# Optimization experiments

Measured on AMD Instinct MI355X. Metric: run time of the kernel, lower is better.

Reference implementation:

```python
import jax, jax.numpy as jnp
import numpy as np

IN_C, HID_C, OUT_C = 6, 128, 6
B, H, W = 8, 256, 256


def _make_weight(key, oc, ic):
    return jax.random.normal(key, (oc, ic, 5), dtype=jnp.float32) / np.sqrt(ic * 5)


def setup_inputs() -> dict:
    key = jax.random.key(0)
    ks = jax.random.split(key, 5)
    x = jax.random.normal(ks[0], (B, IN_C, H, W), dtype=jnp.float32)
    return {
        "x": x,
        "w1": _make_weight(ks[1], HID_C, IN_C),
        "b1": jnp.zeros((HID_C,), jnp.float32),
        "w2": _make_weight(ks[2], HID_C, HID_C),
        "b2": jnp.zeros((HID_C,), jnp.float32),
        "w3": _make_weight(ks[3], HID_C, HID_C),
        "b3": jnp.zeros((HID_C,), jnp.float32),
        "w4": _make_weight(ks[4], OUT_C, HID_C),
        "b4": jnp.zeros((OUT_C,), jnp.float32),
    }


def cross_conv(x, w, b):
    # w: [oc, ic, 5] -> dense 3x3 kernel with 5-point cross stencil
    oc, ic, _ = w.shape
    k = jnp.zeros((oc, ic, 3, 3), dtype=w.dtype)
    k = k.at[:, :, 1, 1].set(w[:, :, 0])  # center
    k = k.at[:, :, 0, 1].set(w[:, :, 1])  # up
    k = k.at[:, :, 2, 1].set(w[:, :, 2])  # down
    k = k.at[:, :, 1, 0].set(w[:, :, 3])  # left
    k = k.at[:, :, 1, 2].set(w[:, :, 4])  # right
    y = jax.lax.conv_general_dilated(
        x, k, window_strides=(1, 1), padding="SAME",
        dimension_numbers=("NCHW", "OIHW", "NCHW"))
    return y + b[None, :, None, None]


def reference(x, w1, b1, w2, b2, w3, b3, w4, b4):
    h = jax.nn.relu(cross_conv(x, w1, b1))
    h = jax.nn.relu(cross_conv(h, w2, b2))
    h = jax.nn.relu(cross_conv(h, w3, b3))
    return cross_conv(h, w4, b4)
```

## Files before the change

kernel.cpp:

```cpp
#include <hip/hip_runtime.h>


#define BB   8
#define HH   256
#define WW   256

typedef _Float16 f16x8 __attribute__((ext_vector_type(8)));
typedef float    f32x4 __attribute__((ext_vector_type(4)));

__device__ _Float16 W1g[128 * 32];
__device__ _Float16 W2g[20 * 128 * 32];
__device__ _Float16 W3g[20 * 128 * 32];
__device__ _Float16 W4g[5 * 16 * 128];

__global__ void prep(const float* __restrict__ w1, const float* __restrict__ w2,
                     const float* __restrict__ w3, const float* __restrict__ w4)
{
    int idx = blockIdx.x * 256 + threadIdx.x;
    if (idx < 81920) {
        int icb = idx & 31, oc = (idx >> 5) & 127, ks = idx >> 12;
        int tap = ks >> 2, ic = (ks & 3) * 32 + icb;
        W2g[idx] = (_Float16)w2[(oc * 128 + ic) * 5 + tap];
    } else if (idx < 163840) {
        int k = idx - 81920;
        int icb = k & 31, oc = (k >> 5) & 127, ks = k >> 12;
        int tap = ks >> 2, ic = (ks & 3) * 32 + icb;
        W3g[k] = (_Float16)w3[(oc * 128 + ic) * 5 + tap];
    } else if (idx < 174080) {
        int k = idx - 163840;
        int t = k / 2048, oc = (k >> 7) & 15, ic = k & 127;
        W4g[k] = (_Float16)((oc < 6) ? w4[(oc * 128 + ic) * 5 + t] : 0.f);
    } else if (idx < 178176) {
        int k = idx - 174080;
        int kk = k & 31, oc = k >> 5;
        float v = 0.f;
        if (kk < 30) {
            int tap = (kk * 43) >> 8;
            int ic = kk - 6 * tap;
            v = w1[(oc * 6 + ic) * 5 + tap];
        }
        W1g[k] = (_Float16)v;
    }
}

template<int HALF, bool EDGE>
__device__ __forceinline__ void g1_stage(const float* __restrict__ xb,
                                         _Float16* __restrict__ Ap,
                                         int px, int gi0, int gj0)
{
#pragma unroll
    for (int it = 0; it < 15; ++it) {
        const int k = 2 * it + HALF;
        const int tap = k / 6, ic = k - 6 * tap;
        const int DI = (tap == 1) ? -1 : ((tap == 2) ? 1 : 0);
        const int DJ = (tap == 3) ? -1 : ((tap == 4) ? 1 : 0);
        const float* sp = xb + ic * 65536 + DI * 256 + DJ;
        float v;
        if (EDGE) {
            const int gi = gi0 + DI, gj = gj0 + DJ;
            v = ((unsigned)gi < 256u && (unsigned)gj < 256u) ? *sp : 0.f;
        } else {
            v = *sp;
        }
        Ap[px * 40 + k] = (_Float16)v;
    }
    Ap[px * 40 + 30 + HALF] = (_Float16)0.f;
}

__global__ __launch_bounds__(256, 3) void g1(
    const float* __restrict__ x, const float* __restrict__ bias,
    _Float16* __restrict__ outp)
{
    __shared__ _Float16 Ap[128 * 40];
    const int tid = threadIdx.x;
    const int j0 = blockIdx.x * 16, i0 = blockIdx.y * 8, b = blockIdx.z;
    const int px = tid & 127, half = tid >> 7;
    const int pr = px >> 4, pp = px & 15;
    const bool edge = (blockIdx.y == 0) | (blockIdx.y == 31) |
                      (blockIdx.x == 0) | (blockIdx.x == 15);
    const int gi0 = i0 + pr, gj0 = j0 + pp;
    const float* xb = x + (size_t)b * 6 * 65536 + gi0 * 256 + gj0;

    if (edge) {
        if (half == 0) g1_stage<0, true >(xb, Ap, px, gi0, gj0);
        else           g1_stage<1, true >(xb, Ap, px, gi0, gj0);
    } else {
        if (half == 0) g1_stage<0, false>(xb, Ap, px, gi0, gj0);
        else           g1_stage<1, false>(xb, Ap, px, gi0, gj0);
    }
    __syncthreads();

    const int lane = tid & 63, w = tid >> 6, l16 = lane & 15, quad = lane >> 4;
    f32x4 acc[2][8] = {};
    f16x8 a0 = *(const f16x8*)&Ap[((2 * w + 0) * 16 + l16) * 40 + quad * 8];
    f16x8 a1 = *(const f16x8*)&Ap[((2 * w + 1) * 16 + l16) * 40 + quad * 8];
#pragma unroll
    for (int nf = 0; nf < 8; ++nf) {
        f16x8 bf = *(const f16x8*)&W1g[(nf * 16 + l16) * 32 + quad * 8];
        acc[0][nf] = __builtin_amdgcn_mfma_f32_16x16x32_f16(a0, bf, acc[0][nf], 0, 0, 0);
        acc[1][nf] = __builtin_amdgcn_mfma_f32_16x16x32_f16(a1, bf, acc[1][nf], 0, 0, 0);
    }
#pragma unroll
    for (int mf = 0; mf < 2; ++mf) {
        const size_t rowb = ((size_t)b * 256 + i0 + 2 * w + mf) * 256 + j0;
#pragma unroll
        for (int nf = 0; nf < 8; ++nf) {
            const float bv = bias[nf * 16 + l16];
#pragma unroll
            for (int r = 0; r < 4; ++r)
                outp[(rowb + quad * 4 + r) * 128 + nf * 16 + l16] =
                    (_Float16)fmaxf(acc[mf][nf][r] + bv, 0.f);
        }
    }
}

template<int LAYER>
__global__ __launch_bounds__(256, 3) void gmid(
    const _Float16* __restrict__ in, const float* __restrict__ bias,
    _Float16* __restrict__ outp)
{
    const _Float16* wt = (LAYER == 2) ? W2g : W3g;
    __shared__ __align__(16) _Float16 Al[180 * 128];
    const int tid = threadIdx.x;
    const int lane = tid & 63, w = tid >> 6;
    const int j0 = blockIdx.x * 16, i0 = blockIdx.y * 8, b = blockIdx.z;
    const bool top = (blockIdx.y == 0), bot = (blockIdx.y == 31);
    const bool left = (blockIdx.x == 0), right = (blockIdx.x == 15);

    {
        const int pxl = lane & 15;
#pragma unroll
        for (int k = 0; k < 12; ++k) {
            const int m = w + 4 * k;
            if (m < 45) {
                const int s = 4 * m + (lane >> 4);
                const int r = (s * 114) >> 11;
                const int p = s - 18 * r;
                int gi = i0 - 1 + r; gi = gi < 0 ? 0 : (gi > 255 ? 255 : gi);
                int gj = j0 - 1 + p; gj = gj < 0 ? 0 : (gj > 255 ? 255 : gj);
                const _Float16* src = in + (((size_t)(b * 256 + gi)) * 256 + gj) * 128
                                         + ((pxl ^ (s & 7)) << 3);
                __builtin_amdgcn_global_load_lds(
                    (const __attribute__((address_space(1))) void*)src,
                    (__attribute__((address_space(3))) void*)(Al + m * 512),
                    16, 0, 0);
            }
        }
    }
    __syncthreads();
    if (top | bot | left | right) {
#pragma unroll
        for (int pass = 0; pass < 2; ++pass) {
            const int gidx = (tid >> 3) + 32 * pass, c = tid & 7;
            int sid = -1;
            if (gidx < 18)      { if (top)   sid = gidx; }
            else if (gidx < 36) { if (bot)   sid = 162 + gidx - 18; }
            else if (gidx < 46) { if (left)  sid = (gidx - 36) * 18; }
            else if (gidx < 56) { if (right) sid = (gidx - 46) * 18 + 17; }
            if (sid >= 0) {
                const f16x8 z = {};
                *(f16x8*)(Al + sid * 128 + c * 16)     = z;
                *(f16x8*)(Al + sid * 128 + c * 16 + 8) = z;
            }
        }
        __syncthreads();
    }

    const int l16 = lane & 15, quad = lane >> 4;
    const int mg = w & 1, ng = w >> 1;
    const int r0 = mg * 4;
    const int n0 = ng * 64;

    const _Float16* wb = wt + (size_t)(n0 + l16) * 32 + quad * 8;

    f32x4 acc[4][4] = {};
    const int DR[5] = {1, 0, 2, 1, 1}, DP[5] = {1, 1, 1, 0, 2};

    auto lda = [&](int ks, int r) -> f16x8 {
        const int tap = ks >> 2, kc = ks & 3;
        const int s = (DR[tap] + r0 + r) * 18 + DP[tap] + l16;
        const int ch = (kc * 4 + quad) ^ (s & 7);
        return *(const f16x8*)&Al[s * 128 + ch * 8];
    };

    f16x8 bc[4], bn[4], ac[4], an[4];
#pragma unroll
    for (int nf = 0; nf < 4; ++nf) bc[nf] = *(const f16x8*)(wb + nf * 512);
#pragma unroll
    for (int r = 0; r < 4; ++r) ac[r] = lda(0, r);

#pragma unroll
    for (int ks = 0; ks < 20; ++ks) {
        if (ks < 19) {
#pragma unroll
            for (int nf = 0; nf < 4; ++nf)
                bn[nf] = *(const f16x8*)(wb + (size_t)(ks + 1) * 4096 + nf * 512);
#pragma unroll
            for (int r = 0; r < 4; ++r) an[r] = lda(ks + 1, r);
        }
        __builtin_amdgcn_s_setprio(1);
#pragma unroll
        for (int r = 0; r < 4; ++r)
#pragma unroll
            for (int nf = 0; nf < 4; ++nf)
                acc[r][nf] = __builtin_amdgcn_mfma_f32_16x16x32_f16(
                    ac[r], bc[nf], acc[r][nf], 0, 0, 0);
        __builtin_amdgcn_s_setprio(0);
#pragma unroll
        for (int nf = 0; nf < 4; ++nf) bc[nf] = bn[nf];
#pragma unroll
        for (int r = 0; r < 4; ++r) ac[r] = an[r];
    }

#pragma unroll
    for (int r = 0; r < 4; ++r) {
        const size_t rowb = ((size_t)b * 256 + i0 + r0 + r) * 256 + j0;
#pragma unroll
        for (int nf = 0; nf < 4; ++nf) {
            const float bv = bias[n0 + nf * 16 + l16];
#pragma unroll
            for (int vi = 0; vi < 4; ++vi)
                outp[(rowb + quad * 4 + vi) * 128 + n0 + nf * 16 + l16] =
                    (_Float16)fmaxf(acc[r][nf][vi] + bv, 0.f);
        }
    }
}

__global__ __launch_bounds__(256, 3) void g4(
    const _Float16* __restrict__ in, const float* __restrict__ bias,
    float* __restrict__ outp)
{
    __shared__ __align__(16) _Float16 Al[180 * 128];
    const int tid = threadIdx.x;
    const int lane = tid & 63, w = tid >> 6;
    const int j0 = blockIdx.x * 16, i0 = blockIdx.y * 8, b = blockIdx.z;
    const bool top = (blockIdx.y == 0), bot = (blockIdx.y == 31);
    const bool left = (blockIdx.x == 0), right = (blockIdx.x == 15);

    {
        const int pxl = lane & 15;
#pragma unroll
        for (int k = 0; k < 12; ++k) {
            const int m = w + 4 * k;
            if (m < 45) {
                const int s = 4 * m + (lane >> 4);
                const int r = (s * 114) >> 11;
                const int p = s - 18 * r;
                int gi = i0 - 1 + r; gi = gi < 0 ? 0 : (gi > 255 ? 255 : gi);
                int gj = j0 - 1 + p; gj = gj < 0 ? 0 : (gj > 255 ? 255 : gj);
                const _Float16* src = in + (((size_t)(b * 256 + gi)) * 256 + gj) * 128
                                         + ((pxl ^ (s & 7)) << 3);
                __builtin_amdgcn_global_load_lds(
                    (const __attribute__((address_space(1))) void*)src,
                    (__attribute__((address_space(3))) void*)(Al + m * 512),
                    16, 0, 0);
            }
        }
    }
    __syncthreads();
    if (top | bot | left | right) {
#pragma unroll
        for (int pass = 0; pass < 2; ++pass) {
            const int gidx = (tid >> 3) + 32 * pass, c = tid & 7;
            int sid = -1;
            if (gidx < 18)      { if (top)   sid = gidx; }
            else if (gidx < 36) { if (bot)   sid = 162 + gidx - 18; }
            else if (gidx < 46) { if (left)  sid = (gidx - 36) * 18; }
            else if (gidx < 56) { if (right) sid = (gidx - 46) * 18 + 17; }
            if (sid >= 0) {
                const f16x8 z = {};
                *(f16x8*)(Al + sid * 128 + c * 16)     = z;
                *(f16x8*)(Al + sid * 128 + c * 16 + 8) = z;
            }
        }
        __syncthreads();
    }

    const int l16 = lane & 15, quad = lane >> 4;
    const int DR[5] = {1, 0, 2, 1, 1}, DP[5] = {1, 1, 1, 0, 2};

    auto lda = [&](int ks, int row) -> f16x8 {
        const int tap = ks >> 2, kc = ks & 3;
        const int s = (DR[tap] + row) * 18 + DP[tap] + l16;
        const int ch = (kc * 4 + quad) ^ (s & 7);
        return *(const f16x8*)&Al[s * 128 + ch * 8];
    };
    auto ldb = [&](int ks) -> f16x8 {
        const int tap = ks >> 2, kc = ks & 3;
        return *(const f16x8*)&W4g[(size_t)(tap * 16 + l16) * 128 + kc * 32 + quad * 8];
    };

    f32x4 acc[2] = {};
    f16x8 bfc = ldb(0), bfn;
    f16x8 afc0 = lda(0, 2 * w), afc1 = lda(0, 2 * w + 1), afn0, afn1;
#pragma unroll
    for (int ks = 0; ks < 20; ++ks) {
        if (ks < 19) {
            bfn  = ldb(ks + 1);
            afn0 = lda(ks + 1, 2 * w);
            afn1 = lda(ks + 1, 2 * w + 1);
        }
        __builtin_amdgcn_s_setprio(1);
        acc[0] = __builtin_amdgcn_mfma_f32_16x16x32_f16(afc0, bfc, acc[0], 0, 0, 0);
        acc[1] = __builtin_amdgcn_mfma_f32_16x16x32_f16(afc1, bfc, acc[1], 0, 0, 0);
        __builtin_amdgcn_s_setprio(0);
        bfc = bfn; afc0 = afn0; afc1 = afn1;
    }

    if (l16 < 6) {
        const float bb = bias[l16];
#pragma unroll
        for (int f = 0; f < 2; ++f) {
            const int i = i0 + 2 * w + f;
#pragma unroll
            for (int vi = 0; vi < 4; ++vi) {
                int jj = j0 + quad * 4 + vi;
                outp[(((size_t)b * 6 + l16) << 16) + i * 256 + jj] = acc[f][vi] + bb;
            }
        }
    }
}

extern "C" void kernel_launch(void* const* d_in, const int* in_sizes, int n_in,
                              void* d_out, int out_size, void* d_ws, size_t ws_size,
                              hipStream_t stream) {
    const float* x  = (const float*)d_in[0];
    const float* w1 = (const float*)d_in[1];
    const float* b1 = (const float*)d_in[2];
    const float* w2 = (const float*)d_in[3];
    const float* b2 = (const float*)d_in[4];
    const float* w3 = (const float*)d_in[5];
    const float* b3 = (const float*)d_in[6];
    const float* w4 = (const float*)d_in[7];
    const float* b4 = (const float*)d_in[8];
    float* out = (float*)d_out;

    const size_t act = (size_t)BB * HH * WW * 128;
    _Float16* A1 = (_Float16*)d_ws;
    _Float16* A2 = A1 + act;

    prep<<<696, 256, 0, stream>>>(w1, w2, w3, w4);
    dim3 blk(256, 1, 1);
    dim3 gm(16, 32, 8);
    g1<<<gm, blk, 0, stream>>>(x, b1, A1);
    gmid<2><<<gm, blk, 0, stream>>>(A1, b2, A2);
    gmid<3><<<gm, blk, 0, stream>>>(A2, b3, A1);
    g4<<<gm, blk, 0, stream>>>(A1, b4, out);
}
```

Before: 384.2 us.

## Make gmid persistent over four column tiles with register-staged prefetch

Each gmid block now processes four consecutive 16-column tiles instead of one, so the grid shrinks from 16 to 4 blocks along x. The halo tile for the next column is loaded into registers while the current tile's MFMA loop and epilogue run, then written to LDS between barriers. This replaces the async global_load_lds path with register staging and hoists the bias loads out of the tile loop. The aim is to hide global load latency behind compute. The costs are higher register pressure, extra barriers per tile, fewer blocks in flight, and a full halo reload per tile with no reuse of the overlapping columns.

Result: slower. 1.436 ms (+273.8%).

```diff
diff --git a/kernel.cpp b/kernel.cpp
--- a/kernel.cpp
+++ b/kernel.cpp
@@ -123,6 +123,163 @@
     __shared__ __align__(16) _Float16 Al[180 * 128];
     const int tid = threadIdx.x;
     const int lane = tid & 63, w = tid >> 6;
+    const int jh = blockIdx.x, band = blockIdx.y, b = blockIdx.z;
+    const int i0 = band * 8;
+    const bool top = (band == 0), bot = (band == 31);
+
+    auto src_off = [&](int k, int j0t) -> unsigned {
+        const int id = tid + 256 * k, s = id >> 4, c = id & 15;
+        const int r = (s * 114) >> 11, p = s - 18 * r;
+        int gi = i0 - 1 + r; gi = gi < 0 ? 0 : (gi > 255 ? 255 : gi);
+        int gj = j0t - 1 + p; gj = gj < 0 ? 0 : (gj > 255 ? 255 : gj);
+        return (unsigned)((((b * 256 + gi) * 256 + gj) * 128) + ((c ^ (s & 7)) << 3));
+    };
+    auto lds_off = [&](int k) -> int {
+        const int id = tid + 256 * k, s = id >> 4, c = id & 15;
+        return s * 128 + c * 8;
+    };
+
+    f16x8 vst[12];
+#define ISSUE(k, j0t) vst[k] = *(const f16x8*)&in[src_off(k, j0t)]
+#define FLUSH(k)      *(f16x8*)&Al[lds_off(k)] = vst[k]
+
+    auto fixup = [&](bool ftop, bool fbot, bool fl, bool fr) {
+#pragma unroll
+        for (int pass = 0; pass < 2; ++pass) {
+            const int gidx = (tid >> 3) + 32 * pass, c = tid & 7;
+            int sid = -1;
+            if (gidx < 18)      { if (ftop) sid = gidx; }
+            else if (gidx < 36) { if (fbot) sid = 162 + gidx - 18; }
+            else if (gidx < 46) { if (fl)   sid = (gidx - 36) * 18; }
+            else if (gidx < 56) { if (fr)   sid = (gidx - 46) * 18 + 17; }
+            if (sid >= 0) {
+                const f16x8 z = {};
+                *(f16x8*)(Al + sid * 128 + c * 16)     = z;
+                *(f16x8*)(Al + sid * 128 + c * 16 + 8) = z;
+            }
+        }
+    };
+
+    const int l16 = lane & 15, quad = lane >> 4;
+    const int mg = w & 1, ng = w >> 1;
+    const int r0 = mg * 4, n0 = ng * 64;
+    const _Float16* wb = wt + (size_t)(n0 + l16) * 32 + quad * 8;
+    const int DR[5] = {1, 0, 2, 1, 1}, DP[5] = {1, 1, 1, 0, 2};
+    float bv[4];
+#pragma unroll
+    for (int nf = 0; nf < 4; ++nf) bv[nf] = bias[n0 + nf * 16 + l16];
+
+    auto lda = [&](int ks, int r) -> f16x8 {
+        const int tap = ks >> 2, kc = ks & 3;
+        const int s = (DR[tap] + r0 + r) * 18 + DP[tap] + l16;
+        const int ch = (kc * 4 + quad) ^ (s & 7);
+        return *(const f16x8*)&Al[s * 128 + ch * 8];
+    };
+
+    {
+        const int j00 = jh * 64;
+#pragma unroll
+        for (int k = 0; k < 11; ++k) ISSUE(k, j00);
+        if (tid < 64) ISSUE(11, j00);
+#pragma unroll
+        for (int k = 0; k < 11; ++k) FLUSH(k);
+        if (tid < 64) FLUSH(11);
+    }
+    __syncthreads();
+    {
+        const bool fl = (jh == 0);
+        if (top | bot | fl) { fixup(top, bot, fl, false); __syncthreads(); }
+    }
+
+#pragma unroll 1
+    for (int t = 0; t < 4; ++t) {
+        const int j0 = jh * 64 + t * 16;
+        const int j0n = j0 + 16;
+
+        if (t < 3) {
+#pragma unroll
+            for (int k = 0; k < 6; ++k) ISSUE(k, j0n);
+            __builtin_amdgcn_sched_barrier(0);
+        }
+
+        f32x4 acc[4][4] = {};
+        f16x8 bc[4], bn[4], ac[4], an[4];
+#pragma unroll
+        for (int nf = 0; nf < 4; ++nf) bc[nf] = *(const f16x8*)(wb + nf * 512);
+#pragma unroll
+        for (int r = 0; r < 4; ++r) ac[r] = lda(0, r);
+
+#pragma unroll
+        for (int ks = 0; ks < 20; ++ks) {
+            if (ks < 19) {
+#pragma unroll
+                for (int nf = 0; nf < 4; ++nf)
+                    bn[nf] = *(const f16x8*)(wb + (size_t)(ks + 1) * 4096 + nf * 512);
+#pragma unroll
+                for (int r = 0; r < 4; ++r) an[r] = lda(ks + 1, r);
+            }
+            __builtin_amdgcn_s_setprio(1);
+#pragma unroll
+            for (int r = 0; r < 4; ++r)
+#pragma unroll
+                for (int nf = 0; nf < 4; ++nf)
+                    acc[r][nf] = __builtin_amdgcn_mfma_f32_16x16x32_f16(
+                        ac[r], bc[nf], acc[r][nf], 0, 0, 0);
+            __builtin_amdgcn_s_setprio(0);
+#pragma unroll
+            for (int nf = 0; nf < 4; ++nf) bc[nf] = bn[nf];
+#pragma unroll
+            for (int r = 0; r < 4; ++r) ac[r] = an[r];
+        }
+
+#pragma unroll
+        for (int r = 0; r < 2; ++r) {
+            const size_t rowb = ((size_t)b * 256 + i0 + r0 + r) * 256 + j0;
+#pragma unroll
+            for (int nf = 0; nf < 4; ++nf)
+#pragma unroll
+                for (int vi = 0; vi < 4; ++vi)
+                    outp[(rowb + quad * 4 + vi) * 128 + n0 + nf * 16 + l16] =
+                        (_Float16)fmaxf(acc[r][nf][vi] + bv[nf], 0.f);
+        }
+        if (t < 3) {
+#pragma unroll
+            for (int k = 6; k < 11; ++k) ISSUE(k, j0n);
+            if (tid < 64) ISSUE(11, j0n);
+            __builtin_amdgcn_sched_barrier(0);
+        }
+#pragma unroll
+        for (int r = 2; r < 4; ++r) {
+            const size_t rowb = ((size_t)b * 256 + i0 + r0 + r) * 256 + j0;
+#pragma unroll
+            for (int nf = 0; nf < 4; ++nf)
+#pragma unroll
+                for (int vi = 0; vi < 4; ++vi)
+                    outp[(rowb + quad * 4 + vi) * 128 + n0 + nf * 16 + l16] =
+                        (_Float16)fmaxf(acc[r][nf][vi] + bv[nf], 0.f);
+        }
+
+        if (t < 3) {
+            __syncthreads();
+#pragma unroll
+            for (int k = 0; k < 11; ++k) FLUSH(k);
+            if (tid < 64) FLUSH(11);
+            __syncthreads();
+            const bool fr = (jh == 3) && (t + 1 == 3);
+            if (top | bot | fr) { fixup(top, bot, false, fr); __syncthreads(); }
+        }
+    }
+#undef ISSUE
+#undef FLUSH
+}
+
+__global__ __launch_bounds__(256, 3) void g4(
+    const _Float16* __restrict__ in, const float* __restrict__ bias,
+    float* __restrict__ outp)
+{
+    __shared__ __align__(16) _Float16 Al[180 * 128];
+    const int tid = threadIdx.x;
+    const int lane = tid & 63, w = tid >> 6;
     const int j0 = blockIdx.x * 16, i0 = blockIdx.y * 8, b = blockIdx.z;
     const bool top = (blockIdx.y == 0), bot = (blockIdx.y == 31);
     const bool left = (blockIdx.x == 0), right = (blockIdx.x == 15);
@@ -167,116 +324,6 @@
     }
 
     const int l16 = lane & 15, quad = lane >> 4;
-    const int mg = w & 1, ng = w >> 1;
-    const int r0 = mg * 4;
-    const int n0 = ng * 64;
-
-    const _Float16* wb = wt + (size_t)(n0 + l16) * 32 + quad * 8;
-
-    f32x4 acc[4][4] = {};
-    const int DR[5] = {1, 0, 2, 1, 1}, DP[5] = {1, 1, 1, 0, 2};
-
-    auto lda = [&](int ks, int r) -> f16x8 {
-        const int tap = ks >> 2, kc = ks & 3;
-        const int s = (DR[tap] + r0 + r) * 18 + DP[tap] + l16;
-        const int ch = (kc * 4 + quad) ^ (s & 7);
-        return *(const f16x8*)&Al[s * 128 + ch * 8];
-    };
-
-    f16x8 bc[4], bn[4], ac[4], an[4];
-#pragma unroll
-    for (int nf = 0; nf < 4; ++nf) bc[nf] = *(const f16x8*)(wb + nf * 512);
-#pragma unroll
-    for (int r = 0; r < 4; ++r) ac[r] = lda(0, r);
-
-#pragma unroll
-    for (int ks = 0; ks < 20; ++ks) {
-        if (ks < 19) {
-#pragma unroll
-            for (int nf = 0; nf < 4; ++nf)
-                bn[nf] = *(const f16x8*)(wb + (size_t)(ks + 1) * 4096 + nf * 512);
-#pragma unroll
-            for (int r = 0; r < 4; ++r) an[r] = lda(ks + 1, r);
-        }
-        __builtin_amdgcn_s_setprio(1);
-#pragma unroll
-        for (int r = 0; r < 4; ++r)
-#pragma unroll
-            for (int nf = 0; nf < 4; ++nf)
-                acc[r][nf] = __builtin_amdgcn_mfma_f32_16x16x32_f16(
-                    ac[r], bc[nf], acc[r][nf], 0, 0, 0);
-        __builtin_amdgcn_s_setprio(0);
-#pragma unroll
-        for (int nf = 0; nf < 4; ++nf) bc[nf] = bn[nf];
-#pragma unroll
-        for (int r = 0; r < 4; ++r) ac[r] = an[r];
-    }
-
-#pragma unroll
-    for (int r = 0; r < 4; ++r) {
-        const size_t rowb = ((size_t)b * 256 + i0 + r0 + r) * 256 + j0;
-#pragma unroll
-        for (int nf = 0; nf < 4; ++nf) {
-            const float bv = bias[n0 + nf * 16 + l16];
-#pragma unroll
-            for (int vi = 0; vi < 4; ++vi)
-                outp[(rowb + quad * 4 + vi) * 128 + n0 + nf * 16 + l16] =
-                    (_Float16)fmaxf(acc[r][nf][vi] + bv, 0.f);
-        }
-    }
-}
-
-__global__ __launch_bounds__(256, 3) void g4(
-    const _Float16* __restrict__ in, const float* __restrict__ bias,
-    float* __restrict__ outp)
-{
-    __shared__ __align__(16) _Float16 Al[180 * 128];
-    const int tid = threadIdx.x;
-    const int lane = tid & 63, w = tid >> 6;
-    const int j0 = blockIdx.x * 16, i0 = blockIdx.y * 8, b = blockIdx.z;
-    const bool top = (blockIdx.y == 0), bot = (blockIdx.y == 31);
-    const bool left = (blockIdx.x == 0), right = (blockIdx.x == 15);
-
-    {
-        const int pxl = lane & 15;
-#pragma unroll
-        for (int k = 0; k < 12; ++k) {
-            const int m = w + 4 * k;
-            if (m < 45) {
-                const int s = 4 * m + (lane >> 4);
-                const int r = (s * 114) >> 11;
-                const int p = s - 18 * r;
-                int gi = i0 - 1 + r; gi = gi < 0 ? 0 : (gi > 255 ? 255 : gi);
-                int gj = j0 - 1 + p; gj = gj < 0 ? 0 : (gj > 255 ? 255 : gj);
-                const _Float16* src = in + (((size_t)(b * 256 + gi)) * 256 + gj) * 128
-                                         + ((pxl ^ (s & 7)) << 3);
-                __builtin_amdgcn_global_load_lds(
-                    (const __attribute__((address_space(1))) void*)src,
-                    (__attribute__((address_space(3))) void*)(Al + m * 512),
-                    16, 0, 0);
-            }
-        }
-    }
-    __syncthreads();
-    if (top | bot | left | right) {
-#pragma unroll
-        for (int pass = 0; pass < 2; ++pass) {
-            const int gidx = (tid >> 3) + 32 * pass, c = tid & 7;
-            int sid = -1;
-            if (gidx < 18)      { if (top)   sid = gidx; }
-            else if (gidx < 36) { if (bot)   sid = 162 + gidx - 18; }
-            else if (gidx < 46) { if (left)  sid = (gidx - 36) * 18; }
-            else if (gidx < 56) { if (right) sid = (gidx - 46) * 18 + 17; }
-            if (sid >= 0) {
-                const f16x8 z = {};
-                *(f16x8*)(Al + sid * 128 + c * 16)     = z;
-                *(f16x8*)(Al + sid * 128 + c * 16 + 8) = z;
-            }
-        }
-        __syncthreads();
-    }
-
-    const int l16 = lane & 15, quad = lane >> 4;
     const int DR[5] = {1, 0, 2, 1, 1}, DP[5] = {1, 1, 1, 0, 2};
 
     auto lda = [&](int ks, int row) -> f16x8 {
@@ -343,7 +390,7 @@
     dim3 blk(256, 1, 1);
     dim3 gm(16, 32, 8);
     g1<<<gm, blk, 0, stream>>>(x, b1, A1);
-    gmid<2><<<gm, blk, 0, stream>>>(A1, b2, A2);
-    gmid<3><<<gm, blk, 0, stream>>>(A2, b3, A1);
+    gmid<2><<<dim3(4, 32, 8), blk, 0, stream>>>(A1, b2, A2);
+    gmid<3><<<dim3(4, 32, 8), blk, 0, stream>>>(A2, b3, A1);
     g4<<<gm, blk, 0, stream>>>(A1, b4, out);
 }
```

## Make gmid blocks persistent over two batch images, overlapping next staging with epilogue

Applied to the files above, without the earlier changes.

Each gmid block now processes two batch images (b0 and b0+4), so the grid is halved along z. After the MFMA loop for the first image, the block waits for its LDS reads, barriers, and issues the async global-to-LDS loads for the second tile before writing out the first tile's results. This hides part of the halo staging latency behind the epilogue stores and amortizes weight-pointer setup. The cost is half as many blocks (2048 per layer), which lowers parallel slack and tail balance, and relies on manual waitcnt and barrier ordering.

After: 1.025 ms. 167% more time.

```diff
diff --git a/kernel.cpp b/kernel.cpp
--- a/kernel.cpp
+++ b/kernel.cpp
@@ -123,6 +123,137 @@
     __shared__ __align__(16) _Float16 Al[180 * 128];
     const int tid = threadIdx.x;
     const int lane = tid & 63, w = tid >> 6;
+    const int j0 = blockIdx.x * 16, i0 = blockIdx.y * 8, b0 = blockIdx.z;
+    const bool top = (blockIdx.y == 0), bot = (blockIdx.y == 31);
+    const bool left = (blockIdx.x == 0), right = (blockIdx.x == 15);
+    const bool edge = top | bot | left | right;
+    const int pxl = lane & 15;
+
+    auto stage = [&](int bb) {
+#pragma unroll
+        for (int k = 0; k < 12; ++k) {
+            const int m = w + 4 * k;
+            if (m < 45) {
+                const int s = 4 * m + (lane >> 4);
+                const int r = (s * 114) >> 11;
+                const int p = s - 18 * r;
+                int gi = i0 - 1 + r; gi = gi < 0 ? 0 : (gi > 255 ? 255 : gi);
+                int gj = j0 - 1 + p; gj = gj < 0 ? 0 : (gj > 255 ? 255 : gj);
+                const _Float16* src = in + (((size_t)(bb * 256 + gi)) * 256 + gj) * 128
+                                         + ((pxl ^ (s & 7)) << 3);
+                __builtin_amdgcn_global_load_lds(
+                    (const __attribute__((address_space(1))) void*)src,
+                    (__attribute__((address_space(3))) void*)(Al + m * 512),
+                    16, 0, 0);
+            }
+        }
+    };
+
+    auto fixup = [&]() {
+#pragma unroll
+        for (int pass = 0; pass < 2; ++pass) {
+            const int gidx = (tid >> 3) + 32 * pass, c = tid & 7;
+            int sid = -1;
+            if (gidx < 18)      { if (top)   sid = gidx; }
+            else if (gidx < 36) { if (bot)   sid = 162 + gidx - 18; }
+            else if (gidx < 46) { if (left)  sid = (gidx - 36) * 18; }
+            else if (gidx < 56) { if (right) sid = (gidx - 46) * 18 + 17; }
+            if (sid >= 0) {
+                const f16x8 z = {};
+                *(f16x8*)(Al + sid * 128 + c * 16)     = z;
+                *(f16x8*)(Al + sid * 128 + c * 16 + 8) = z;
+            }
+        }
+    };
+
+    const int l16 = lane & 15, quad = lane >> 4;
+    const int mg = w & 1, ng = w >> 1;
+    const int r0 = mg * 4;
+    const int n0 = ng * 64;
+    const _Float16* wb = wt + (size_t)(n0 + l16) * 32 + quad * 8;
+    const int DR[5] = {1, 0, 2, 1, 1}, DP[5] = {1, 1, 1, 0, 2};
+
+    auto lda = [&](int ks, int r) -> f16x8 {
+        const int tap = ks >> 2, kc = ks & 3;
+        const int s = (DR[tap] + r0 + r) * 18 + DP[tap] + l16;
+        const int ch = (kc * 4 + quad) ^ (s & 7);
+        return *(const f16x8*)&Al[s * 128 + ch * 8];
+    };
+
+    stage(b0);
+    __syncthreads();
+    if (edge) { fixup(); __syncthreads(); }
+
+#pragma unroll 1
+    for (int t = 0; t < 2; ++t) {
+        const int b = b0 + 4 * t;
+
+        f32x4 acc[4][4] = {};
+        f16x8 bc[4], bn[4], ac[4], an[4];
+#pragma unroll
+        for (int nf = 0; nf < 4; ++nf) bc[nf] = *(const f16x8*)(wb + nf * 512);
+#pragma unroll
+        for (int r = 0; r < 4; ++r) ac[r] = lda(0, r);
+
+#pragma unroll
+        for (int ks = 0; ks < 20; ++ks) {
+            if (ks < 19) {
+#pragma unroll
+                for (int nf = 0; nf < 4; ++nf)
+                    bn[nf] = *(const f16x8*)(wb + (size_t)(ks + 1) * 4096 + nf * 512);
+#pragma unroll
+                for (int r = 0; r < 4; ++r) an[r] = lda(ks + 1, r);
+            }
+            __builtin_amdgcn_s_setprio(1);
+#pragma unroll
+            for (int r = 0; r < 4; ++r)
+#pragma unroll
+                for (int nf = 0; nf < 4; ++nf)
+                    acc[r][nf] = __builtin_amdgcn_mfma_f32_16x16x32_f16(
+                        ac[r], bc[nf], acc[r][nf], 0, 0, 0);
+            __builtin_amdgcn_s_setprio(0);
+#pragma unroll
+            for (int nf = 0; nf < 4; ++nf) bc[nf] = bn[nf];
+#pragma unroll
+            for (int r = 0; r < 4; ++r) ac[r] = an[r];
+        }
+
+        if (t == 0) {
+            asm volatile("s_waitcnt lgkmcnt(0)" ::: "memory");
+            __builtin_amdgcn_sched_barrier(0);
+            __builtin_amdgcn_s_barrier();
+            stage(b0 + 4);
+        }
+
+#pragma unroll
+        for (int r = 0; r < 4; ++r) {
+            const size_t rowb = ((size_t)b * 256 + i0 + r0 + r) * 256 + j0;
+#pragma unroll
+            for (int nf = 0; nf < 4; ++nf) {
+                const float bv = bias[n0 + nf * 16 + l16];
+#pragma unroll
+                for (int vi = 0; vi < 4; ++vi)
+                    outp[(rowb + quad * 4 + vi) * 128 + n0 + nf * 16 + l16] =
+                        (_Float16)fmaxf(acc[r][nf][vi] + bv, 0.f);
+            }
+        }
+
+        if (t == 0) {
+            asm volatile("s_waitcnt vmcnt(0)" ::: "memory");
+            __builtin_amdgcn_sched_barrier(0);
+            __builtin_amdgcn_s_barrier();
+            if (edge) { fixup(); __syncthreads(); }
+        }
+    }
+}
+
+__global__ __launch_bounds__(256, 3) void g4(
+    const _Float16* __restrict__ in, const float* __restrict__ bias,
+    float* __restrict__ outp)
+{
+    __shared__ __align__(16) _Float16 Al[180 * 128];
+    const int tid = threadIdx.x;
+    const int lane = tid & 63, w = tid >> 6;
     const int j0 = blockIdx.x * 16, i0 = blockIdx.y * 8, b = blockIdx.z;
     const bool top = (blockIdx.y == 0), bot = (blockIdx.y == 31);
     const bool left = (blockIdx.x == 0), right = (blockIdx.x == 15);
@@ -167,116 +298,6 @@
     }
 
     const int l16 = lane & 15, quad = lane >> 4;
-    const int mg = w & 1, ng = w >> 1;
-    const int r0 = mg * 4;
-    const int n0 = ng * 64;
-
-    const _Float16* wb = wt + (size_t)(n0 + l16) * 32 + quad * 8;
-
-    f32x4 acc[4][4] = {};
-    const int DR[5] = {1, 0, 2, 1, 1}, DP[5] = {1, 1, 1, 0, 2};
-
-    auto lda = [&](int ks, int r) -> f16x8 {
-        const int tap = ks >> 2, kc = ks & 3;
-        const int s = (DR[tap] + r0 + r) * 18 + DP[tap] + l16;
-        const int ch = (kc * 4 + quad) ^ (s & 7);
-        return *(const f16x8*)&Al[s * 128 + ch * 8];
-    };
-
-    f16x8 bc[4], bn[4], ac[4], an[4];
-#pragma unroll
-    for (int nf = 0; nf < 4; ++nf) bc[nf] = *(const f16x8*)(wb + nf * 512);
-#pragma unroll
-    for (int r = 0; r < 4; ++r) ac[r] = lda(0, r);
-
-#pragma unroll
-    for (int ks = 0; ks < 20; ++ks) {
-        if (ks < 19) {
-#pragma unroll
-            for (int nf = 0; nf < 4; ++nf)
-                bn[nf] = *(const f16x8*)(wb + (size_t)(ks + 1) * 4096 + nf * 512);
-#pragma unroll
-            for (int r = 0; r < 4; ++r) an[r] = lda(ks + 1, r);
-        }
-        __builtin_amdgcn_s_setprio(1);
-#pragma unroll
-        for (int r = 0; r < 4; ++r)
-#pragma unroll
-            for (int nf = 0; nf < 4; ++nf)
-                acc[r][nf] = __builtin_amdgcn_mfma_f32_16x16x32_f16(
-                    ac[r], bc[nf], acc[r][nf], 0, 0, 0);
-        __builtin_amdgcn_s_setprio(0);
-#pragma unroll
-        for (int nf = 0; nf < 4; ++nf) bc[nf] = bn[nf];
-#pragma unroll
-        for (int r = 0; r < 4; ++r) ac[r] = an[r];
-    }
-
-#pragma unroll
-    for (int r = 0; r < 4; ++r) {
-        const size_t rowb = ((size_t)b * 256 + i0 + r0 + r) * 256 + j0;
-#pragma unroll
-        for (int nf = 0; nf < 4; ++nf) {
-            const float bv = bias[n0 + nf * 16 + l16];
-#pragma unroll
-            for (int vi = 0; vi < 4; ++vi)
-                outp[(rowb + quad * 4 + vi) * 128 + n0 + nf * 16 + l16] =
-                    (_Float16)fmaxf(acc[r][nf][vi] + bv, 0.f);
-        }
-    }
-}
-
-__global__ __launch_bounds__(256, 3) void g4(
-    const _Float16* __restrict__ in, const float* __restrict__ bias,
-    float* __restrict__ outp)
-{
-    __shared__ __align__(16) _Float16 Al[180 * 128];
-    const int tid = threadIdx.x;
-    const int lane = tid & 63, w = tid >> 6;
-    const int j0 = blockIdx.x * 16, i0 = blockIdx.y * 8, b = blockIdx.z;
-    const bool top = (blockIdx.y == 0), bot = (blockIdx.y == 31);
-    const bool left = (blockIdx.x == 0), right = (blockIdx.x == 15);
-
-    {
-        const int pxl = lane & 15;
-#pragma unroll
-        for (int k = 0; k < 12; ++k) {
-            const int m = w + 4 * k;
-            if (m < 45) {
-                const int s = 4 * m + (lane >> 4);
-                const int r = (s * 114) >> 11;
-                const int p = s - 18 * r;
-                int gi = i0 - 1 + r; gi = gi < 0 ? 0 : (gi > 255 ? 255 : gi);
-                int gj = j0 - 1 + p; gj = gj < 0 ? 0 : (gj > 255 ? 255 : gj);
-                const _Float16* src = in + (((size_t)(b * 256 + gi)) * 256 + gj) * 128
-                                         + ((pxl ^ (s & 7)) << 3);
-                __builtin_amdgcn_global_load_lds(
-                    (const __attribute__((address_space(1))) void*)src,
-                    (__attribute__((address_space(3))) void*)(Al + m * 512),
-                    16, 0, 0);
-            }
-        }
-    }
-    __syncthreads();
-    if (top | bot | left | right) {
-#pragma unroll
-        for (int pass = 0; pass < 2; ++pass) {
-            const int gidx = (tid >> 3) + 32 * pass, c = tid & 7;
-            int sid = -1;
-            if (gidx < 18)      { if (top)   sid = gidx; }
-            else if (gidx < 36) { if (bot)   sid = 162 + gidx - 18; }
-            else if (gidx < 46) { if (left)  sid = (gidx - 36) * 18; }
-            else if (gidx < 56) { if (right) sid = (gidx - 46) * 18 + 17; }
-            if (sid >= 0) {
-                const f16x8 z = {};
-                *(f16x8*)(Al + sid * 128 + c * 16)     = z;
-                *(f16x8*)(Al + sid * 128 + c * 16 + 8) = z;
-            }
-        }
-        __syncthreads();
-    }
-
-    const int l16 = lane & 15, quad = lane >> 4;
     const int DR[5] = {1, 0, 2, 1, 1}, DP[5] = {1, 1, 1, 0, 2};
 
     auto lda = [&](int ks, int row) -> f16x8 {
@@ -343,7 +364,7 @@
     dim3 blk(256, 1, 1);
     dim3 gm(16, 32, 8);
     g1<<<gm, blk, 0, stream>>>(x, b1, A1);
-    gmid<2><<<gm, blk, 0, stream>>>(A1, b2, A2);
-    gmid<3><<<gm, blk, 0, stream>>>(A2, b3, A1);
+    gmid<2><<<dim3(16, 32, 4), blk, 0, stream>>>(A1, b2, A2);
+    gmid<3><<<dim3(16, 32, 4), blk, 0, stream>>>(A2, b3, A1);
     g4<<<gm, blk, 0, stream>>>(A1, b4, out);
 }
```
